# Kernel optimization log

Hardware: AMD Instinct MI355X
Metric: run time of the kernel (lower is better)

The kernel has to match this reference:

```python
import jax, jax.numpy as jnp
import numpy as np

N_TX, N_CARD, N_MERCH = 200000, 50000, 10000
E = 200000
TX_IN, EMB, H = 128, 64, 128
N_LAYERS, N_ETYPES = 2, 4  # etypes: 0 card->tx, 1 tx->card, 2 merch->tx, 3 tx->merch


def setup_inputs() -> dict:
    key = jax.random.key(0)
    ks = jax.random.split(key, 24)
    s = 0.05
    inp = {
        "tx_x": jax.random.normal(ks[0], (N_TX, TX_IN), jnp.float32),
        "card_ids": jnp.arange(N_CARD, dtype=jnp.int64),
        "merch_ids": jnp.arange(N_MERCH, dtype=jnp.int64),
        "e_card": jax.random.randint(ks[1], (E,), 0, N_CARD),
        "e_tx_c": jnp.arange(E, dtype=jnp.int64),
        "e_merch": jax.random.randint(ks[2], (E,), 0, N_MERCH),
        "e_tx_m": jnp.arange(E, dtype=jnp.int64),
        # parameters
        "card_emb": jax.random.normal(ks[3], (N_CARD, EMB), jnp.float32) * s,
        "merch_emb": jax.random.normal(ks[4], (N_MERCH, EMB), jnp.float32) * s,
        "card_proj_W": jax.random.normal(ks[5], (EMB, H), jnp.float32) * s,
        "card_proj_b": jnp.zeros((H,), jnp.float32),
        "merch_proj_W": jax.random.normal(ks[6], (EMB, H), jnp.float32) * s,
        "merch_proj_b": jnp.zeros((H,), jnp.float32),
        "tx_W": jax.random.normal(ks[7], (TX_IN, H), jnp.float32) * s,
        "tx_b": jnp.zeros((H,), jnp.float32),
        "conv_Wl": jax.random.normal(ks[8], (N_LAYERS, N_ETYPES, H, H), jnp.float32) * s,
        "conv_bl": jnp.zeros((N_LAYERS, N_ETYPES, H), jnp.float32),
        "conv_Wr": jax.random.normal(ks[9], (N_LAYERS, N_ETYPES, H, H), jnp.float32) * s,
        "h1_W": jax.random.normal(ks[10], (H, H), jnp.float32) * s,
        "h1_b": jnp.zeros((H,), jnp.float32),
        "h2_W": jax.random.normal(ks[11], (H, 1), jnp.float32) * s,
        "h2_b": jnp.zeros((1,), jnp.float32),
    }
    return inp


def _sage(x_src, x_dst, src, dst, Wl, bl, Wr, n_dst):
    # PyG SAGEConv: mean-aggregate neighbor features, then lin_l(agg)+lin_r(x_dst)
    agg = jax.ops.segment_sum(x_src[src], dst, num_segments=n_dst)
    cnt = jax.ops.segment_sum(jnp.ones((src.shape[0],), x_src.dtype), dst, num_segments=n_dst)
    mean = agg / jnp.maximum(cnt, 1.0)[:, None]
    return mean @ Wl + bl + x_dst @ Wr


def reference(tx_x, card_ids, merch_ids, e_card, e_tx_c, e_merch, e_tx_m,
              card_emb, merch_emb, card_proj_W, card_proj_b, merch_proj_W, merch_proj_b,
              tx_W, tx_b, conv_Wl, conv_bl, conv_Wr, h1_W, h1_b, h2_W, h2_b):
    # input encoders (dropout inactive at eval)
    h_tx = jax.nn.relu(tx_x @ tx_W + tx_b)
    h_card = card_emb[card_ids] @ card_proj_W + card_proj_b
    h_merch = merch_emb[merch_ids] @ merch_proj_W + merch_proj_b

    for l in range(N_LAYERS):
        Wl, bl, Wr = conv_Wl[l], conv_bl[l], conv_Wr[l]
        # HeteroConv aggr='sum' across edge types sharing a dst type
        o_tx = (_sage(h_card, h_tx, e_card, e_tx_c, Wl[0], bl[0], Wr[0], N_TX)
                + _sage(h_merch, h_tx, e_merch, e_tx_m, Wl[2], bl[2], Wr[2], N_TX))
        o_card = _sage(h_tx, h_card, e_tx_c, e_card, Wl[1], bl[1], Wr[1], N_CARD)
        o_merch = _sage(h_tx, h_merch, e_tx_m, e_merch, Wl[3], bl[3], Wr[3], N_MERCH)
        h_tx, h_card, h_merch = jax.nn.relu(o_tx), jax.nn.relu(o_card), jax.nn.relu(o_merch)

    logits = (jax.nn.relu(h_tx @ h1_W + h1_b) @ h2_W + h2_b).reshape(-1)
    return logits
```

## Files before the change

### kernel.cpp

```cpp
#include <hip/hip_runtime.h>


#define N_TX    200000
#define N_CARD  50000
#define N_MERCH 10000
#define NE      200000

typedef __attribute__((ext_vector_type(8))) short short8;
typedef __attribute__((ext_vector_type(4))) float f32x4;

__device__ inline unsigned short f2b(float f) {
    unsigned u = __builtin_bit_cast(unsigned, f);
    unsigned r = (u + 0x7fffu + ((u >> 16) & 1u)) >> 16;
    return (unsigned short)r;
}
__device__ inline float b2f(unsigned short s) {
    return __builtin_bit_cast(float, (unsigned)s << 16);
}

__global__ __launch_bounds__(256, 2) void mfma_gemm(
    const void* __restrict__ A1, int a1_f32, const int* __restrict__ rowIdx1,
    int K1, const unsigned short* __restrict__ WT1,
    const void* __restrict__ A2, int K2, const unsigned short* __restrict__ WT2,
    const float* __restrict__ bias,
    const unsigned short* __restrict__ P1, const int* __restrict__ I1,
    const unsigned short* __restrict__ P2, const int* __restrict__ I2,
    int do_relu, const float* __restrict__ h2W, const float* __restrict__ h2b,
    void* __restrict__ OUT, int M)
{
    __shared__ unsigned short WTs[128 * 136];
    const int tid  = threadIdx.x;
    const int wave = tid >> 6;
    const int lane = tid & 63;
    const int quad = lane >> 4;
    const int l15  = lane & 15;
    const int base = blockIdx.x * 128;

    f32x4 acc[2][8];
#pragma unroll
    for (int mt = 0; mt < 2; ++mt)
#pragma unroll
        for (int nt = 0; nt < 8; ++nt)
            acc[mt][nt] = (f32x4){0.f, 0.f, 0.f, 0.f};

    for (int pass = 0; pass < 2; ++pass) {
        const void* A = (pass == 0) ? A1 : A2;
        if (!A) break;
        const int K = (pass == 0) ? K1 : K2;
        const unsigned short* WTg = (pass == 0) ? WT1 : WT2;
        const int* rIdx = (pass == 0) ? rowIdx1 : nullptr;
        const int a_f32 = (pass == 0) ? a1_f32 : 0;
        const int stride = K + 8;
        const int nkk = K >> 5;
        const int ksh = (K == 128) ? 7 : 6;

        __syncthreads();
        for (int i = tid * 8; i < (K << 7); i += 2048) {
            int row = i >> ksh;
            int off = i & (K - 1);
            *reinterpret_cast<short8*>(&WTs[row * stride + off]) =
                *reinterpret_cast<const short8*>(WTg + i);
        }
        __syncthreads();

        short8 af[2][4];
#pragma unroll
        for (int mt = 0; mt < 2; ++mt) {
            int r = base + wave * 32 + mt * 16 + l15;
            int rc = (r < M) ? r : 0;
            int ar = rIdx ? rIdx[rc] : rc;
            if (a_f32) {
                const float* ap = (const float*)A + (size_t)ar * K + quad * 8;
#pragma unroll
                for (int kk = 0; kk < 4; ++kk) if (kk < nkk) {
                    float4 u = *reinterpret_cast<const float4*>(ap + kk * 32);
                    float4 v = *reinterpret_cast<const float4*>(ap + kk * 32 + 4);
                    short8 t;
                    t[0] = (short)f2b(u.x); t[1] = (short)f2b(u.y);
                    t[2] = (short)f2b(u.z); t[3] = (short)f2b(u.w);
                    t[4] = (short)f2b(v.x); t[5] = (short)f2b(v.y);
                    t[6] = (short)f2b(v.z); t[7] = (short)f2b(v.w);
                    af[mt][kk] = t;
                }
            } else {
                const unsigned short* ap =
                    (const unsigned short*)A + (size_t)ar * K + quad * 8;
#pragma unroll
                for (int kk = 0; kk < 4; ++kk) if (kk < nkk)
                    af[mt][kk] = *reinterpret_cast<const short8*>(ap + kk * 32);
            }
        }

#pragma unroll
        for (int nt = 0; nt < 8; ++nt) {
            short8 bf[4];
            const unsigned short* bp = &WTs[(nt * 16 + l15) * stride + quad * 8];
#pragma unroll
            for (int kk = 0; kk < 4; ++kk) if (kk < nkk)
                bf[kk] = *reinterpret_cast<const short8*>(bp + kk * 32);
#pragma unroll
            for (int mt = 0; mt < 2; ++mt)
#pragma unroll
                for (int kk = 0; kk < 4; ++kk) if (kk < nkk)
                    acc[mt][nt] = __builtin_amdgcn_mfma_f32_16x16x32_bf16(
                        af[mt][kk], bf[kk], acc[mt][nt], 0, 0, 0);
        }
    }

    float bias_v[8], h2wv[8];
#pragma unroll
    for (int nt = 0; nt < 8; ++nt) {
        int col = nt * 16 + l15;
        bias_v[nt] = bias ? bias[col] : 0.f;
        h2wv[nt]   = h2W  ? h2W[col]  : 0.f;
    }
    unsigned short* OUTb = (unsigned short*)OUT;
    float* OUTf = (float*)OUT;
#pragma unroll
    for (int mt = 0; mt < 2; ++mt) {
        int rbase = base + wave * 32 + mt * 16 + quad * 4;
#pragma unroll
        for (int reg = 0; reg < 4; ++reg) {
            int r = rbase + reg;
            bool valid = r < M;
            int rc = valid ? r : 0;
            size_t i1 = P1 ? (size_t)I1[rc] * 128 : 0;
            size_t i2 = P2 ? (size_t)I2[rc] * 128 : 0;
            float hsum = 0.f;
#pragma unroll
            for (int nt = 0; nt < 8; ++nt) {
                int col = nt * 16 + l15;
                float o = acc[mt][nt][reg] + bias_v[nt];
                if (P1) o += b2f(P1[i1 + col]);
                if (P2) o += b2f(P2[i2 + col]);
                if (do_relu) o = fmaxf(o, 0.f);
                if (h2W) hsum += o * h2wv[nt];
                else if (valid) OUTb[(size_t)r * 128 + col] = f2b(o);
            }
            if (h2W) {
                hsum += __shfl_xor(hsum, 1);
                hsum += __shfl_xor(hsum, 2);
                hsum += __shfl_xor(hsum, 4);
                hsum += __shfl_xor(hsum, 8);
                if (l15 == 0 && valid) OUTf[r] = hsum + h2b[0];
            }
        }
    }
}

__global__ __launch_bounds__(256) void convert_weights(
    const float* __restrict__ tx_W, const float* __restrict__ card_proj_W,
    const float* __restrict__ merch_proj_W, const float* __restrict__ h1_W,
    const float* __restrict__ conv_Wl, const float* __restrict__ conv_Wr,
    const float* __restrict__ conv_bl,
    unsigned short* __restrict__ WT, float* __restrict__ bsum)
{
    int job = blockIdx.y;
    int K = 128;
    const float* src = nullptr;
    const float* src2 = nullptr;
    if (job == 0) src = tx_W;
    else if (job == 1) { src = card_proj_W; K = 64; }
    else if (job == 2) { src = merch_proj_W; K = 64; }
    else if (job == 3) src = h1_W;
    else {
        int l = (job - 4) / 7, e = (job - 4) % 7;
        const float* Wl = conv_Wl + (size_t)l * 4 * 16384;
        const float* Wr = conv_Wr + (size_t)l * 4 * 16384;
        switch (e) {
            case 0: src = Wl; break;
            case 1: src = Wl + 16384; break;
            case 2: src = Wl + 2 * 16384; break;
            case 3: src = Wl + 3 * 16384; break;
            case 4: src = Wr + 16384; break;
            case 5: src = Wr + 3 * 16384; break;
            default:
                src = Wr; src2 = Wr + 2 * 16384;
                if (blockIdx.x == 0 && threadIdx.x < 128) {
                    const float* bl = conv_bl + (size_t)l * 4 * 128;
                    bsum[l * 128 + threadIdx.x] =
                        bl[threadIdx.x] + bl[2 * 128 + threadIdx.x];
                }
                break;
        }
    }
    int e = blockIdx.x * 256 + threadIdx.x;
    if (e < (K << 7)) {
        int n = (K == 128) ? (e >> 7) : (e >> 6);
        int k = e & (K - 1);
        float v = src[(size_t)k * 128 + n];
        if (src2) v += src2[(size_t)k * 128 + n];
        WT[(size_t)job * 16384 + n * K + k] = f2b(v);
    }
}

__global__ __launch_bounds__(256) void hist_kernel(
    const int* __restrict__ e_card, const int* __restrict__ e_merch,
    int* __restrict__ hist_c, int* __restrict__ hist_m, int E)
{
    int i = blockIdx.x * 256 + threadIdx.x;
    if (i < E) {
        atomicAdd(&hist_c[e_card[i]], 1);
        atomicAdd(&hist_m[e_merch[i]], 1);
    }
}

__global__ __launch_bounds__(1024) void scan2_kernel(
    const int* __restrict__ hist_c, int* __restrict__ offs_c, int* __restrict__ cur_c, int nc,
    const int* __restrict__ hist_m, int* __restrict__ offs_m, int* __restrict__ cur_m, int nm)
{
    const int* hist = (blockIdx.x == 0) ? hist_c : hist_m;
    int* offs = (blockIdx.x == 0) ? offs_c : offs_m;
    int* cursor = (blockIdx.x == 0) ? cur_c : cur_m;
    int n = (blockIdx.x == 0) ? nc : nm;
    __shared__ int wsum[16];
    __shared__ int s_carry;
    const int tid = threadIdx.x, lane = tid & 63, wid = tid >> 6;
    if (tid == 0) s_carry = 0;
    __syncthreads();
    for (int base = 0; base < n; base += 1024) {
        int i = base + tid;
        int v = (i < n) ? hist[i] : 0;
        int x = v;
#pragma unroll
        for (int d = 1; d < 64; d <<= 1) {
            int t = __shfl_up(x, d);
            if (lane >= d) x += t;
        }
        if (lane == 63) wsum[wid] = x;
        __syncthreads();
        if (wid == 0) {
            int y = (lane < 16) ? wsum[lane] : 0;
#pragma unroll
            for (int d = 1; d < 16; d <<= 1) {
                int t = __shfl_up(y, d);
                if (lane >= d) y += t;
            }
            if (lane < 16) wsum[lane] = y;
        }
        __syncthreads();
        int wbase = (wid > 0) ? wsum[wid - 1] : 0;
        int excl = s_carry + wbase + x - v;
        if (i < n) { offs[i] = excl; cursor[i] = excl; }
        __syncthreads();
        if (tid == 0) s_carry += wsum[15];
        __syncthreads();
    }
    if (threadIdx.x == 0) offs[n] = s_carry;
}

__global__ __launch_bounds__(256) void place_kernel(
    const int* __restrict__ e_card, const int* __restrict__ e_tx_c,
    const int* __restrict__ e_merch, const int* __restrict__ e_tx_m,
    int* __restrict__ cur_c, int* __restrict__ eidx_c,
    int* __restrict__ cur_m, int* __restrict__ eidx_m, int E)
{
    int i = blockIdx.x * 256 + threadIdx.x;
    if (i < E) {
        int pc = atomicAdd(&cur_c[e_card[i]], 1);
        eidx_c[pc] = e_tx_c[i];
        int pm = atomicAdd(&cur_m[e_merch[i]], 1);
        eidx_m[pm] = e_tx_m[i];
    }
}

__global__ __launch_bounds__(256) void gather_mean(
    const unsigned short* __restrict__ h_src, const int* __restrict__ offs,
    const int* __restrict__ eidx, unsigned short* __restrict__ out_mean, int n_dst)
{
    const int lane = threadIdx.x & 63;
    const int d = blockIdx.x * 4 + (threadIdx.x >> 6);
    if (d >= n_dst) return;
    const int s = offs[d], e = offs[d + 1];
    float a0 = 0.f, a1 = 0.f;
    for (int p = s; p < e; ++p) {
        int tx = eidx[p];
        unsigned v = *reinterpret_cast<const unsigned*>(
            h_src + (size_t)tx * 128 + lane * 2);
        a0 += b2f((unsigned short)(v & 0xffff));
        a1 += b2f((unsigned short)(v >> 16));
    }
    const float inv = (e > s) ? 1.0f / (float)(e - s) : 0.f;
    unsigned o = ((unsigned)f2b(a1 * inv) << 16) | f2b(a0 * inv);
    *reinterpret_cast<unsigned*>(out_mean + (size_t)d * 128 + lane * 2) = o;
}

extern "C" void kernel_launch(void* const* d_in, const int* in_sizes, int n_in,
                              void* d_out, int out_size, void* d_ws, size_t ws_size,
                              hipStream_t stream)
{
    const float* tx_x        = (const float*)d_in[0];
    const int*   card_ids    = (const int*)d_in[1];
    const int*   merch_ids   = (const int*)d_in[2];
    const int*   e_card      = (const int*)d_in[3];
    const int*   e_tx_c      = (const int*)d_in[4];
    const int*   e_merch     = (const int*)d_in[5];
    const int*   e_tx_m      = (const int*)d_in[6];
    const float* card_emb    = (const float*)d_in[7];
    const float* merch_emb   = (const float*)d_in[8];
    const float* card_proj_W = (const float*)d_in[9];
    const float* card_proj_b = (const float*)d_in[10];
    const float* merch_proj_W= (const float*)d_in[11];
    const float* merch_proj_b= (const float*)d_in[12];
    const float* tx_W        = (const float*)d_in[13];
    const float* tx_b        = (const float*)d_in[14];
    const float* conv_Wl     = (const float*)d_in[15];
    const float* conv_bl     = (const float*)d_in[16];
    const float* conv_Wr     = (const float*)d_in[17];
    const float* h1_W        = (const float*)d_in[18];
    const float* h1_b        = (const float*)d_in[19];
    const float* h2_W        = (const float*)d_in[20];
    const float* h2_b        = (const float*)d_in[21];

    char* wsb = (char*)d_ws;
    auto alloc = [&](size_t bytes) {
        char* p = wsb; wsb += (bytes + 255) & ~(size_t)255; return p;
    };
    unsigned short* h_tx       = (unsigned short*)alloc((size_t)N_TX * 128 * 2);
    unsigned short* h_card     = (unsigned short*)alloc((size_t)N_CARD * 128 * 2);
    unsigned short* h_merch    = (unsigned short*)alloc((size_t)N_MERCH * 128 * 2);
    unsigned short* p_card     = (unsigned short*)alloc((size_t)N_CARD * 128 * 2);
    unsigned short* p_merch    = (unsigned short*)alloc((size_t)N_MERCH * 128 * 2);
    unsigned short* mean_card  = (unsigned short*)alloc((size_t)N_CARD * 128 * 2);
    unsigned short* mean_merch = (unsigned short*)alloc((size_t)N_MERCH * 128 * 2);
    unsigned short* WT         = (unsigned short*)alloc((size_t)18 * 16384 * 2);
    float* bsum = (float*)alloc(2 * 128 * 4);
    int* hist_c = (int*)alloc((size_t)(N_CARD + N_MERCH) * 4);
    int* hist_m = hist_c + N_CARD;
    int* offs_c = (int*)alloc((size_t)(N_CARD + 1) * 4);
    int* cur_c  = (int*)alloc((size_t)N_CARD * 4);
    int* eidx_c = (int*)alloc((size_t)NE * 4);
    int* offs_m = (int*)alloc((size_t)(N_MERCH + 1) * 4);
    int* cur_m  = (int*)alloc((size_t)N_MERCH * 4);
    int* eidx_m = (int*)alloc((size_t)NE * 4);

    auto WTj = [&](int job) { return WT + (size_t)job * 16384; };

    auto gemm = [&](const void* A1, int a1f32, const int* ri, int K1,
                    const unsigned short* W1, const void* A2, int K2,
                    const unsigned short* W2, const float* bias,
                    const unsigned short* P1, const int* I1,
                    const unsigned short* P2, const int* I2, int relu,
                    const float* h2w, const float* h2bb, void* out, int M) {
        mfma_gemm<<<dim3((M + 127) / 128), dim3(256), 0, stream>>>(
            A1, a1f32, ri, K1, W1, A2, K2, W2, bias, P1, I1, P2, I2, relu,
            h2w, h2bb, out, M);
    };

    convert_weights<<<dim3(64, 18), dim3(256), 0, stream>>>(
        tx_W, card_proj_W, merch_proj_W, h1_W, conv_Wl, conv_Wr, conv_bl,
        WT, bsum);
    hipMemsetAsync(hist_c, 0, (size_t)(N_CARD + N_MERCH) * 4, stream);
    hist_kernel<<<dim3((NE + 255) / 256), dim3(256), 0, stream>>>(
        e_card, e_merch, hist_c, hist_m, NE);
    scan2_kernel<<<dim3(2), dim3(1024), 0, stream>>>(
        hist_c, offs_c, cur_c, N_CARD, hist_m, offs_m, cur_m, N_MERCH);
    place_kernel<<<dim3((NE + 255) / 256), dim3(256), 0, stream>>>(
        e_card, e_tx_c, e_merch, e_tx_m, cur_c, eidx_c, cur_m, eidx_m, NE);

    gemm(tx_x, 1, nullptr, 128, WTj(0), nullptr, 0, nullptr, tx_b,
         nullptr, nullptr, nullptr, nullptr, 1, nullptr, nullptr, h_tx, N_TX);
    gemm(card_emb, 1, card_ids, 64, WTj(1), nullptr, 0, nullptr, card_proj_b,
         nullptr, nullptr, nullptr, nullptr, 0, nullptr, nullptr, h_card, N_CARD);
    gemm(merch_emb, 1, merch_ids, 64, WTj(2), nullptr, 0, nullptr, merch_proj_b,
         nullptr, nullptr, nullptr, nullptr, 0, nullptr, nullptr, h_merch, N_MERCH);

    for (int l = 0; l < 2; ++l) {
        const float* bl = conv_bl + (size_t)l * 4 * 128;
        int j = 4 + l * 7;

        gather_mean<<<dim3((N_CARD + 3) / 4), dim3(256), 0, stream>>>(
            h_tx, offs_c, eidx_c, mean_card, N_CARD);
        gather_mean<<<dim3((N_MERCH + 3) / 4), dim3(256), 0, stream>>>(
            h_tx, offs_m, eidx_m, mean_merch, N_MERCH);

        gemm(h_card, 0, nullptr, 128, WTj(j + 0), nullptr, 0, nullptr, nullptr,
             nullptr, nullptr, nullptr, nullptr, 0, nullptr, nullptr, p_card, N_CARD);
        gemm(h_merch, 0, nullptr, 128, WTj(j + 2), nullptr, 0, nullptr, nullptr,
             nullptr, nullptr, nullptr, nullptr, 0, nullptr, nullptr, p_merch, N_MERCH);

        gemm(mean_card, 0, nullptr, 128, WTj(j + 1), h_card, 128, WTj(j + 4),
             bl + 1 * 128, nullptr, nullptr, nullptr, nullptr, 1,
             nullptr, nullptr, h_card, N_CARD);
        gemm(mean_merch, 0, nullptr, 128, WTj(j + 3), h_merch, 128, WTj(j + 5),
             bl + 3 * 128, nullptr, nullptr, nullptr, nullptr, 1,
             nullptr, nullptr, h_merch, N_MERCH);

        gemm(h_tx, 0, nullptr, 128, WTj(j + 6), nullptr, 0, nullptr,
             bsum + l * 128, p_card, e_card, p_merch, e_merch, 1,
             nullptr, nullptr, h_tx, N_TX);
    }

    gemm(h_tx, 0, nullptr, 128, WTj(3), nullptr, 0, nullptr, h1_b,
         nullptr, nullptr, nullptr, nullptr, 1, h2_W, h2_b, d_out, N_TX);
}
```

Before: 812.6 us.

## Stage A tiles through LDS and restage epilogue for coalesced vector I/O

The GEMM kernel now loads the A tile (with optional row gather and fp32-to-bf16 conversion) cooperatively into shared memory using row-contiguous vector loads, replacing per-lane strided fragment loads from global memory. The epilogue writes accumulators to shared memory, then re-reads them so each thread handles 4 contiguous columns. This makes the neighbour-feature adds, output stores and the fused h2 dot product coalesced vector accesses. It doubles LDS use per block, which may reduce occupancy, and adds extra barriers.

```diff
diff --git a/kernel.cpp b/kernel.cpp
--- a/kernel.cpp
+++ b/kernel.cpp
@@ -7,6 +7,7 @@
 #define NE      200000
 
 typedef __attribute__((ext_vector_type(8))) short short8;
+typedef __attribute__((ext_vector_type(4))) short short4v;
 typedef __attribute__((ext_vector_type(4))) float f32x4;
 
 __device__ inline unsigned short f2b(float f) {
@@ -28,7 +29,11 @@
     int do_relu, const float* __restrict__ h2W, const float* __restrict__ h2b,
     void* __restrict__ OUT, int M)
 {
-    __shared__ unsigned short WTs[128 * 136];
+    __shared__ __align__(16) char smem[2 * 128 * 136 * 2];
+    unsigned short* As = (unsigned short*)smem;
+    unsigned short* Ws = (unsigned short*)(smem + 128 * 136 * 2);
+    float* Os = (float*)smem;
+
     const int tid  = threadIdx.x;
     const int wave = tid >> 6;
     const int lane = tid & 63;
@@ -52,49 +57,64 @@
         const int a_f32 = (pass == 0) ? a1_f32 : 0;
         const int stride = K + 8;
         const int nkk = K >> 5;
-        const int ksh = (K == 128) ? 7 : 6;
-
-        __syncthreads();
-        for (int i = tid * 8; i < (K << 7); i += 2048) {
-            int row = i >> ksh;
-            int off = i & (K - 1);
-            *reinterpret_cast<short8*>(&WTs[row * stride + off]) =
-                *reinterpret_cast<const short8*>(WTg + i);
+        const int klog = (K == 128) ? 7 : 6;
+        const int kmask = K - 1;
+
+        __syncthreads();
+
+        if (a_f32) {
+            const float* Af = (const float*)A;
+            const int iters = (K == 128) ? 16 : 8;
+            for (int it = 0; it < iters; ++it) {
+                int u = tid * 4 + it * 1024;
+                int row = u >> klog;
+                int col = u & kmask;
+                int gr = base + row;
+                int ar = (gr < M) ? (rIdx ? rIdx[gr] : gr) : 0;
+                float4 v = *reinterpret_cast<const float4*>(Af + (size_t)ar * K + col);
+                short4v t;
+                t[0] = (short)f2b(v.x); t[1] = (short)f2b(v.y);
+                t[2] = (short)f2b(v.z); t[3] = (short)f2b(v.w);
+                *reinterpret_cast<short4v*>(&As[row * stride + col]) = t;
+            }
+        } else {
+            const unsigned short* Ab = (const unsigned short*)A;
+            const int iters = (K == 128) ? 8 : 4;
+            for (int it = 0; it < iters; ++it) {
+                int u = tid * 8 + it * 2048;
+                int row = u >> klog;
+                int col = u & kmask;
+                int gr = base + row;
+                int ar = (gr < M) ? (rIdx ? rIdx[gr] : gr) : 0;
+                *reinterpret_cast<short8*>(&As[row * stride + col]) =
+                    *reinterpret_cast<const short8*>(Ab + (size_t)ar * K + col);
+            }
+        }
+        {
+            const int iters = (K == 128) ? 8 : 4;
+            for (int it = 0; it < iters; ++it) {
+                int u = tid * 8 + it * 2048;
+                int row = u >> klog;
+                int col = u & kmask;
+                *reinterpret_cast<short8*>(&Ws[row * stride + col]) =
+                    *reinterpret_cast<const short8*>(WTg + u);
+            }
         }
         __syncthreads();
 
         short8 af[2][4];
 #pragma unroll
         for (int mt = 0; mt < 2; ++mt) {
-            int r = base + wave * 32 + mt * 16 + l15;
-            int rc = (r < M) ? r : 0;
-            int ar = rIdx ? rIdx[rc] : rc;
-            if (a_f32) {
-                const float* ap = (const float*)A + (size_t)ar * K + quad * 8;
-#pragma unroll
-                for (int kk = 0; kk < 4; ++kk) if (kk < nkk) {
-                    float4 u = *reinterpret_cast<const float4*>(ap + kk * 32);
-                    float4 v = *reinterpret_cast<const float4*>(ap + kk * 32 + 4);
-                    short8 t;
-                    t[0] = (short)f2b(u.x); t[1] = (short)f2b(u.y);
-                    t[2] = (short)f2b(u.z); t[3] = (short)f2b(u.w);
-                    t[4] = (short)f2b(v.x); t[5] = (short)f2b(v.y);
-                    t[6] = (short)f2b(v.z); t[7] = (short)f2b(v.w);
-                    af[mt][kk] = t;
-                }
-            } else {
-                const unsigned short* ap =
-                    (const unsigned short*)A + (size_t)ar * K + quad * 8;
-#pragma unroll
-                for (int kk = 0; kk < 4; ++kk) if (kk < nkk)
-                    af[mt][kk] = *reinterpret_cast<const short8*>(ap + kk * 32);
-            }
-        }
-
+            const unsigned short* ap =
+                &As[(wave * 32 + mt * 16 + l15) * stride + quad * 8];
+#pragma unroll
+            for (int kk = 0; kk < 4; ++kk) if (kk < nkk)
+                af[mt][kk] = *reinterpret_cast<const short8*>(ap + kk * 32);
+        }
 #pragma unroll
         for (int nt = 0; nt < 8; ++nt) {
             short8 bf[4];
-            const unsigned short* bp = &WTs[(nt * 16 + l15) * stride + quad * 8];
+            const unsigned short* bp = &Ws[(nt * 16 + l15) * stride + quad * 8];
 #pragma unroll
             for (int kk = 0; kk < 4; ++kk) if (kk < nkk)
                 bf[kk] = *reinterpret_cast<const short8*>(bp + kk * 32);
@@ -107,43 +127,64 @@
         }
     }
 
-    float bias_v[8], h2wv[8];
-#pragma unroll
-    for (int nt = 0; nt < 8; ++nt) {
-        int col = nt * 16 + l15;
-        bias_v[nt] = bias ? bias[col] : 0.f;
-        h2wv[nt]   = h2W  ? h2W[col]  : 0.f;
-    }
+    float bias_v[8];
+#pragma unroll
+    for (int nt = 0; nt < 8; ++nt)
+        bias_v[nt] = bias ? bias[nt * 16 + l15] : 0.f;
+
+    __syncthreads();
+#pragma unroll
+    for (int mt = 0; mt < 2; ++mt) {
+        int rbase = wave * 32 + mt * 16 + quad * 4;
+#pragma unroll
+        for (int reg = 0; reg < 4; ++reg)
+#pragma unroll
+            for (int nt = 0; nt < 8; ++nt)
+                Os[(rbase + reg) * 132 + nt * 16 + l15] =
+                    acc[mt][nt][reg] + bias_v[nt];
+    }
+    __syncthreads();
+
+    const int col4 = (tid & 31) * 4;
+    float4 h2w4 = make_float4(0.f, 0.f, 0.f, 0.f);
+    if (h2W) h2w4 = *reinterpret_cast<const float4*>(h2W + col4);
     unsigned short* OUTb = (unsigned short*)OUT;
     float* OUTf = (float*)OUT;
-#pragma unroll
-    for (int mt = 0; mt < 2; ++mt) {
-        int rbase = base + wave * 32 + mt * 16 + quad * 4;
-#pragma unroll
-        for (int reg = 0; reg < 4; ++reg) {
-            int r = rbase + reg;
-            bool valid = r < M;
-            int rc = valid ? r : 0;
-            size_t i1 = P1 ? (size_t)I1[rc] * 128 : 0;
-            size_t i2 = P2 ? (size_t)I2[rc] * 128 : 0;
-            float hsum = 0.f;
-#pragma unroll
-            for (int nt = 0; nt < 8; ++nt) {
-                int col = nt * 16 + l15;
-                float o = acc[mt][nt][reg] + bias_v[nt];
-                if (P1) o += b2f(P1[i1 + col]);
-                if (P2) o += b2f(P2[i2 + col]);
-                if (do_relu) o = fmaxf(o, 0.f);
-                if (h2W) hsum += o * h2wv[nt];
-                else if (valid) OUTb[(size_t)r * 128 + col] = f2b(o);
-            }
-            if (h2W) {
-                hsum += __shfl_xor(hsum, 1);
-                hsum += __shfl_xor(hsum, 2);
-                hsum += __shfl_xor(hsum, 4);
-                hsum += __shfl_xor(hsum, 8);
-                if (l15 == 0 && valid) OUTf[r] = hsum + h2b[0];
-            }
+
+#pragma unroll
+    for (int it = 0; it < 16; ++it) {
+        int row = it * 8 + (tid >> 5);
+        int gr = base + row;
+        bool valid = gr < M;
+        int grc = valid ? gr : 0;
+        float4 o = *reinterpret_cast<const float4*>(&Os[row * 132 + col4]);
+        if (P1) {
+            size_t ix = (size_t)(I1 ? I1[grc] : grc) * 128 + col4;
+            short4v p = *reinterpret_cast<const short4v*>(P1 + ix);
+            o.x += b2f((unsigned short)p[0]); o.y += b2f((unsigned short)p[1]);
+            o.z += b2f((unsigned short)p[2]); o.w += b2f((unsigned short)p[3]);
+        }
+        if (P2) {
+            size_t ix = (size_t)(I2 ? I2[grc] : grc) * 128 + col4;
+            short4v p = *reinterpret_cast<const short4v*>(P2 + ix);
+            o.x += b2f((unsigned short)p[0]); o.y += b2f((unsigned short)p[1]);
+            o.z += b2f((unsigned short)p[2]); o.w += b2f((unsigned short)p[3]);
+        }
+        if (do_relu) {
+            o.x = fmaxf(o.x, 0.f); o.y = fmaxf(o.y, 0.f);
+            o.z = fmaxf(o.z, 0.f); o.w = fmaxf(o.w, 0.f);
+        }
+        if (h2W) {
+            float s = o.x * h2w4.x + o.y * h2w4.y + o.z * h2w4.z + o.w * h2w4.w;
+            s += __shfl_xor(s, 1);  s += __shfl_xor(s, 2);
+            s += __shfl_xor(s, 4);  s += __shfl_xor(s, 8);
+            s += __shfl_xor(s, 16);
+            if ((tid & 31) == 0 && valid) OUTf[gr] = s + h2b[0];
+        } else if (valid) {
+            short4v t;
+            t[0] = (short)f2b(o.x); t[1] = (short)f2b(o.y);
+            t[2] = (short)f2b(o.z); t[3] = (short)f2b(o.w);
+            *reinterpret_cast<short4v*>(OUTb + (size_t)gr * 128 + col4) = t;
         }
     }
 }
```

New measurement: 825.3 us. No clear change (+1.6%).
